# Kernel optimization log

Measured on AMD Instinct MI355X. Metric: run time of the kernel, lower is better.

Reference implementation:

```python
import jax, jax.numpy as jnp
import numpy as np

N_NODES, N_EDGES, IN_DIM, HID, N_FEAT_CLOSE, N_GRAPHS = 100000, 1600000, 128, 64, 5, 512


def _glorot(k, shape):
    lim = float(np.sqrt(6.0 / (shape[0] + shape[1])))
    return jax.random.uniform(k, shape, jnp.float32, -lim, lim)


def setup_inputs() -> dict:
    key = jax.random.key(0)
    ks = jax.random.split(key, 16)
    x = jax.random.normal(ks[0], (N_NODES, IN_DIM), jnp.float32)
    edge_index = jax.random.randint(ks[1], (2, N_EDGES), 0, N_NODES, jnp.int32)
    closeness = jax.random.uniform(ks[2], (N_NODES, N_FEAT_CLOSE), jnp.float32)
    batch = jnp.sort(jax.random.randint(ks[3], (N_NODES,), 0, N_GRAPHS, jnp.int32))
    return {
        'x': x, 'edge_index': edge_index, 'closeness': closeness, 'batch': batch,
        'num_graphs': N_GRAPHS,
        'W1': _glorot(ks[4], (IN_DIM, HID)), 'b1': jnp.zeros((HID,), jnp.float32),
        'W2': _glorot(ks[5], (HID, HID)), 'b2': jnp.zeros((HID,), jnp.float32),
        'W3': _glorot(ks[6], (HID, HID)), 'b3': jnp.zeros((HID,), jnp.float32),
        'Wc': _glorot(ks[7], (N_FEAT_CLOSE, 1)), 'bc': jnp.zeros((1,), jnp.float32),
        'Wa1': _glorot(ks[8], (HID, 16)), 'ba1': jnp.zeros((16,), jnp.float32),
        'Wa2': _glorot(ks[9], (16, 1)), 'ba2': jnp.zeros((1,), jnp.float32),
    }


def reference(x, edge_index, closeness, batch, num_graphs, W1, b1, W2, b2, W3, b3, Wc, bc, Wa1, ba1, Wa2, ba2):
    src, dst = edge_index[0], edge_index[1]
    N = x.shape[0]
    # GCN symmetric normalization with implicit self-loops (weight 1)
    deg = jax.ops.segment_sum(jnp.ones(src.shape, x.dtype), dst, num_segments=N) + 1.0
    dinv = jax.lax.rsqrt(deg)
    norm = dinv[src] * dinv[dst]  # [E]
    self_norm = (dinv * dinv)[:, None]  # 1/deg, self-loop coefficient

    def gcn(h, W, b):
        h = h @ W  # [N, hid]
        agg = jax.ops.segment_sum(h[src] * norm[:, None], dst, num_segments=N)
        return jax.nn.relu(agg + h * self_norm + b)

    h = gcn(x, W1, b1)
    h = gcn(h, W2, b2)
    h = gcn(h, W3, b3)

    # per-graph softmax over closeness scores, scaled by graph size
    s = closeness @ Wc + bc  # [N,1]
    smax = jax.ops.segment_max(s, batch, num_segments=num_graphs)
    e = jnp.exp(s - smax[batch])
    ssum = jax.ops.segment_sum(e, batch, num_segments=num_graphs)
    counts = jax.ops.segment_sum(jnp.ones((N,), x.dtype), batch, num_segments=num_graphs)
    w = (e / ssum[batch]) * counts[batch][:, None]  # [N,1]

    # weighted per-graph max pooling, then tiny MLP per graph
    pooled = jax.ops.segment_max(w * h, batch, num_segments=num_graphs)  # [G,64]
    a = jax.nn.relu(pooled @ Wa1 + ba1)
    return a @ Wa2 + ba2  # [G,1]
```

## Files before the change

### kernel.cpp

```cpp
#include <hip/hip_runtime.h>

#define N_NODESC 100000
#define N_EDGESC 1600000
#define IN_DIMC 128
#define HIDC 64
#define N_GRAPHSC 512
#define PAD_DEG 64


__global__ void zero_bounds_kernel(int* __restrict__ cntR, const int* __restrict__ batch,
                                   int* __restrict__ gstart) {
  int i = blockIdx.x * blockDim.x + threadIdx.x;
  if (i >= N_NODESC) return;
  cntR[i] = 0;
  cntR[N_NODESC + i] = 0;
  cntR[2 * N_NODESC + i] = 0;
  cntR[3 * N_NODESC + i] = 0;
  int b = batch[i];
  int prev = (i == 0) ? -1 : batch[i - 1];
  for (int g = prev + 1; g <= b; ++g) gstart[g] = i;
  if (i == N_NODESC - 1)
    for (int g = b + 1; g <= N_GRAPHSC; ++g) gstart[g] = N_NODESC;
}

__global__ void deg_kernel(const int* __restrict__ dstv, int* __restrict__ cntR,
                           int* __restrict__ slot) {
  int e4 = (blockIdx.x * blockDim.x + threadIdx.x) * 4;
  if (e4 >= N_EDGESC) return;
  int4 d = *(const int4*)(dstv + e4);
  int4 s;
  s.x = atomicAdd(&cntR[d.x], 1);
  s.y = atomicAdd(&cntR[N_NODESC + d.y], 1);
  s.z = atomicAdd(&cntR[2 * N_NODESC + d.z], 1);
  s.w = atomicAdd(&cntR[3 * N_NODESC + d.w], 1);
  *(int4*)(slot + e4) = s;
}

__global__ void off_dinv_kernel(const int* __restrict__ cntR, int* __restrict__ offR,
                                int* __restrict__ cnt, float* __restrict__ dinv) {
  int i = blockIdx.x * blockDim.x + threadIdx.x;
  if (i >= N_NODESC) return;
  int c0 = cntR[i];
  int c1 = cntR[N_NODESC + i];
  int c2 = cntR[2 * N_NODESC + i];
  int c3 = cntR[3 * N_NODESC + i];
  offR[i] = c0;
  offR[N_NODESC + i] = c0 + c1;
  offR[2 * N_NODESC + i] = c0 + c1 + c2;
  int tot = c0 + c1 + c2 + c3;
  cnt[i] = tot;
  dinv[i] = rsqrtf((float)tot + 1.0f);
}

__global__ void fill_pad_kernel(const int* __restrict__ srcv, const int* __restrict__ dstv,
                                const int* __restrict__ slot, const int* __restrict__ offR,
                                int* __restrict__ csr_pad) {
  int e4 = (blockIdx.x * blockDim.x + threadIdx.x) * 4;
  if (e4 >= N_EDGESC) return;
  int4 s = *(const int4*)(srcv + e4);
  int4 d = *(const int4*)(dstv + e4);
  int4 sl = *(const int4*)(slot + e4);
  int p0 = sl.x;
  int p1 = offR[d.y] + sl.y;
  int p2 = offR[N_NODESC + d.z] + sl.z;
  int p3 = offR[2 * N_NODESC + d.w] + sl.w;
  if (p0 < PAD_DEG) __builtin_nontemporal_store(s.x, &csr_pad[d.x * PAD_DEG + p0]);
  if (p1 < PAD_DEG) __builtin_nontemporal_store(s.y, &csr_pad[d.y * PAD_DEG + p1]);
  if (p2 < PAD_DEG) __builtin_nontemporal_store(s.z, &csr_pad[d.z * PAD_DEG + p2]);
  if (p3 < PAD_DEG) __builtin_nontemporal_store(s.w, &csr_pad[d.w * PAD_DEG + p3]);
}


#define GT_M 128
#define XS_LD 132
#define GT_BLOCKS ((N_NODESC + GT_M - 1) / GT_M)

template <int KT>
__global__ void __launch_bounds__(256, 3)
gemm_tile_kernel(const float* __restrict__ X, const float* __restrict__ W,
                 const float* __restrict__ dinv, float* __restrict__ T) {
  __shared__ float xs[64 * XS_LD];
  __shared__ float ws[64 * 64];
  int t = threadIdx.x;
  int base = blockIdx.x * GT_M;
  int r0 = (t >> 4) * 8;
  int c0 = (t & 15) * 4;
  float acc[8][4];
#pragma unroll
  for (int i = 0; i < 8; ++i)
#pragma unroll
    for (int j = 0; j < 4; ++j) acc[i][j] = 0.f;

  int kq = (t & 15) * 4;
  int rr = t >> 4;

  for (int kb = 0; kb < KT; kb += 64) {
    if (kb) __syncthreads();
#pragma unroll
    for (int it = 0; it < 8; ++it) {
      int r = rr + it * 16;
      int grow = base + r;
      if (grow >= N_NODESC) grow = N_NODESC - 1;
      float4 q = *(const float4*)(X + (size_t)grow * KT + kb + kq);
      xs[(kq + 0) * XS_LD + r] = q.x;
      xs[(kq + 1) * XS_LD + r] = q.y;
      xs[(kq + 2) * XS_LD + r] = q.z;
      xs[(kq + 3) * XS_LD + r] = q.w;
    }
#pragma unroll
    for (int it = 0; it < 4; ++it) {
      int idx = (it * 256 + t) * 4;
      *(float4*)(ws + idx) = *(const float4*)(W + (size_t)kb * HIDC + idx);
    }
    __syncthreads();
#pragma unroll 8
    for (int k = 0; k < 64; ++k) {
      float4 xa = *(const float4*)(xs + k * XS_LD + r0);
      float4 xb = *(const float4*)(xs + k * XS_LD + r0 + 4);
      float4 wf = *(const float4*)(ws + k * 64 + c0);
      float xf[8] = {xa.x, xa.y, xa.z, xa.w, xb.x, xb.y, xb.z, xb.w};
      float wv[4] = {wf.x, wf.y, wf.z, wf.w};
#pragma unroll
      for (int i = 0; i < 8; ++i)
#pragma unroll
        for (int j = 0; j < 4; ++j) acc[i][j] = fmaf(xf[i], wv[j], acc[i][j]);
    }
  }
#pragma unroll
  for (int i = 0; i < 8; ++i) {
    int row = base + r0 + i;
    if (row < N_NODESC) {
      float dv = dinv[row];
      float4 o;
      o.x = acc[i][0] * dv;
      o.y = acc[i][1] * dv;
      o.z = acc[i][2] * dv;
      o.w = acc[i][3] * dv;
      *(float4*)(T + (size_t)row * HIDC + c0) = o;
    }
  }
}

__global__ void gather_kernel(const float* __restrict__ ts, const float* __restrict__ dinv,
                              const int* __restrict__ cnt, const int* __restrict__ csr_pad,
                              const float* __restrict__ bias, float* __restrict__ h) {
  int lane = threadIdx.x & 63;
  int node = (blockIdx.x * blockDim.x + threadIdx.x) >> 6;
  if (node >= N_NODESC) return;
  int q = lane >> 4;
  int c = lane & 15;
  int deg = min(cnt[node], PAD_DEG);
  const int* __restrict__ row = csr_pad + node * PAD_DEG;
  const float4* __restrict__ ts4 = (const float4*)ts;
  float4 acc = make_float4(0.f, 0.f, 0.f, 0.f);
  int e = 0;
  for (; e + 16 <= deg; e += 16) {
    int s0 = row[e + q];
    int s1 = row[e + 4 + q];
    int s2 = row[e + 8 + q];
    int s3 = row[e + 12 + q];
    float4 v0 = ts4[s0 * 16 + c];
    float4 v1 = ts4[s1 * 16 + c];
    float4 v2 = ts4[s2 * 16 + c];
    float4 v3 = ts4[s3 * 16 + c];
    acc.x += (v0.x + v1.x) + (v2.x + v3.x);
    acc.y += (v0.y + v1.y) + (v2.y + v3.y);
    acc.z += (v0.z + v1.z) + (v2.z + v3.z);
    acc.w += (v0.w + v1.w) + (v2.w + v3.w);
  }
  for (; e + 4 <= deg; e += 4) {
    int s0 = row[e + q];
    float4 v = ts4[s0 * 16 + c];
    acc.x += v.x;
    acc.y += v.y;
    acc.z += v.z;
    acc.w += v.w;
  }
  if (e < deg && q < deg - e) {
    int s0 = row[e + q];
    float4 v = ts4[s0 * 16 + c];
    acc.x += v.x;
    acc.y += v.y;
    acc.z += v.z;
    acc.w += v.w;
  }
  acc.x += __shfl_xor(acc.x, 16);
  acc.y += __shfl_xor(acc.y, 16);
  acc.z += __shfl_xor(acc.z, 16);
  acc.w += __shfl_xor(acc.w, 16);
  acc.x += __shfl_xor(acc.x, 32);
  acc.y += __shfl_xor(acc.y, 32);
  acc.z += __shfl_xor(acc.z, 32);
  acc.w += __shfl_xor(acc.w, 32);
  if (q == 0) {
    float4 self = ts4[node * 16 + c];
    float4 bv = ((const float4*)bias)[c];
    float dv = dinv[node];
    float4 o;
    o.x = fmaxf(fmaf(acc.x + self.x, dv, bv.x), 0.f);
    o.y = fmaxf(fmaf(acc.y + self.y, dv, bv.y), 0.f);
    o.z = fmaxf(fmaf(acc.z + self.z, dv, bv.z), 0.f);
    o.w = fmaxf(fmaf(acc.w + self.w, dv, bv.w), 0.f);
    ((float4*)h)[node * 16 + c] = o;
  }
}

__global__ void __launch_bounds__(256)
readout_kernel(const float* __restrict__ h, const float* __restrict__ closeness,
               const float* __restrict__ Wc, const float* __restrict__ bc,
               const int* __restrict__ gstart, const float* __restrict__ Wa1,
               const float* __restrict__ ba1, const float* __restrict__ Wa2,
               const float* __restrict__ ba2, float* __restrict__ out) {
  __shared__ float sArr[1024];
  __shared__ float red[256];
  __shared__ float cross[4 * 64];
  int g = blockIdx.x;
  int t = threadIdx.x;
  int n0 = gstart[g], n1 = gstart[g + 1];
  int count = n1 - n0;
  int cap = min(count, 1024);
  float wc0 = Wc[0], wc1 = Wc[1], wc2 = Wc[2], wc3 = Wc[3], wc4 = Wc[4], bcv = bc[0];
  float lmax = -3.4e38f;
  for (int idx = t; idx < cap; idx += 256) {
    const float* c = closeness + (size_t)(n0 + idx) * 5;
    float s = fmaf(c[4], wc4, fmaf(c[3], wc3, fmaf(c[2], wc2, fmaf(c[1], wc1, fmaf(c[0], wc0, bcv)))));
    sArr[idx] = s;
    lmax = fmaxf(lmax, s);
  }
  red[t] = lmax;
  __syncthreads();
  for (int s = 128; s > 0; s >>= 1) {
    if (t < s) red[t] = fmaxf(red[t], red[t + s]);
    __syncthreads();
  }
  float m = red[0];
  __syncthreads();
  float lsum = 0.f;
  for (int idx = t; idx < cap; idx += 256) {
    float e = expf(sArr[idx] - m);
    sArr[idx] = e;
    lsum += e;
  }
  red[t] = lsum;
  __syncthreads();
  for (int s = 128; s > 0; s >>= 1) {
    if (t < s) red[t] += red[t + s];
    __syncthreads();
  }
  float scale = (count > 0) ? ((float)count / red[0]) : 0.f;
  __syncthreads();
  int wv = t >> 6, lane = t & 63;
  float pmax = 0.f;
  for (int idx = wv; idx < cap; idx += 4) {
    float w = sArr[idx] * scale;
    pmax = fmaxf(pmax, w * h[(size_t)(n0 + idx) * HIDC + lane]);
  }
  cross[wv * 64 + lane] = pmax;
  __syncthreads();
  if (wv == 0) {
    float p = fmaxf(fmaxf(cross[lane], cross[64 + lane]),
                    fmaxf(cross[128 + lane], cross[192 + lane]));
    float o = 0.f;
#pragma unroll
    for (int tt = 0; tt < 16; ++tt) {
      float prod = p * Wa1[lane * 16 + tt];
#pragma unroll
      for (int off = 32; off > 0; off >>= 1) prod += __shfl_xor(prod, off);
      float a = fmaxf(prod + ba1[tt], 0.f);
      o += a * Wa2[tt];
    }
    if (lane == 0) out[g] = o + ba2[0];
  }
}


extern "C" void kernel_launch(void* const* d_in, const int* in_sizes, int n_in,
                              void* d_out, int out_size, void* d_ws, size_t ws_size,
                              hipStream_t stream) {
  const float* x = (const float*)d_in[0];
  const int* ei = (const int*)d_in[1];
  const float* closeness = (const float*)d_in[2];
  const int* batch = (const int*)d_in[3];
  const float* W1 = (const float*)d_in[5];
  const float* b1 = (const float*)d_in[6];
  const float* W2 = (const float*)d_in[7];
  const float* b2 = (const float*)d_in[8];
  const float* W3 = (const float*)d_in[9];
  const float* b3 = (const float*)d_in[10];
  const float* Wc = (const float*)d_in[11];
  const float* bc = (const float*)d_in[12];
  const float* Wa1 = (const float*)d_in[13];
  const float* ba1 = (const float*)d_in[14];
  const float* Wa2 = (const float*)d_in[15];
  const float* ba2 = (const float*)d_in[16];
  float* out = (float*)d_out;
  const int* srcv = ei;
  const int* dstv = ei + N_EDGESC;

  char* ws = (char*)d_ws;
  size_t off = 0;
  auto alloc = [&](size_t bytes) -> void* {
    void* p = ws + off;
    off = (off + bytes + 255) & ~(size_t)255;
    return p;
  };
  float* tbuf = (float*)alloc(sizeof(float) * N_NODESC * HIDC);
  float* hbuf = (float*)alloc(sizeof(float) * N_NODESC * HIDC);
  int* csr_pad = (int*)alloc(sizeof(int) * N_NODESC * PAD_DEG);
  int* slot = (int*)alloc(sizeof(int) * N_EDGESC);
  int* cntR = (int*)alloc(sizeof(int) * N_NODESC * 4);
  int* offR = (int*)alloc(sizeof(int) * N_NODESC * 3);
  int* cnt = (int*)alloc(sizeof(int) * N_NODESC);
  float* dinv = (float*)alloc(sizeof(float) * N_NODESC);
  int* gstart = (int*)alloc(sizeof(int) * (N_GRAPHSC + 1));

  const int B = 256;
  int gN = (N_NODESC + B - 1) / B;
  int gE4 = (N_EDGESC / 4 + B - 1) / B;
  int gGather = (N_NODESC * 64) / B;

  zero_bounds_kernel<<<gN, B, 0, stream>>>(cntR, batch, gstart);
  deg_kernel<<<gE4, B, 0, stream>>>(dstv, cntR, slot);
  off_dinv_kernel<<<gN, B, 0, stream>>>(cntR, offR, cnt, dinv);
  fill_pad_kernel<<<gE4, B, 0, stream>>>(srcv, dstv, slot, offR, csr_pad);

  gemm_tile_kernel<IN_DIMC><<<GT_BLOCKS, B, 0, stream>>>(x, W1, dinv, tbuf);
  gather_kernel<<<gGather, B, 0, stream>>>(tbuf, dinv, cnt, csr_pad, b1, hbuf);
  gemm_tile_kernel<HIDC><<<GT_BLOCKS, B, 0, stream>>>(hbuf, W2, dinv, tbuf);
  gather_kernel<<<gGather, B, 0, stream>>>(tbuf, dinv, cnt, csr_pad, b2, hbuf);
  gemm_tile_kernel<HIDC><<<GT_BLOCKS, B, 0, stream>>>(hbuf, W3, dinv, tbuf);
  gather_kernel<<<gGather, B, 0, stream>>>(tbuf, dinv, cnt, csr_pad, b3, hbuf);

  readout_kernel<<<N_GRAPHSC, B, 0, stream>>>(hbuf, closeness, Wc, bc, gstart,
                                              Wa1, ba1, Wa2, ba2, out);
}
```

Baseline: 517.0 us.

## Build CSR in one pass with four interleaved per-replica padded segments

```diff
diff --git a/kernel.cpp b/kernel.cpp
--- a/kernel.cpp
+++ b/kernel.cpp
@@ -5,7 +5,12 @@
 #define IN_DIMC 128
 #define HIDC 64
 #define N_GRAPHSC 512
-#define PAD_DEG 64
+
+#define PAD_SEG 20
+#define ROW_INTS (4 * PAD_SEG)
+
+typedef int v4i __attribute__((ext_vector_type(4)));
+typedef float v4f __attribute__((ext_vector_type(4)));
 
 
 __global__ void zero_bounds_kernel(int* __restrict__ cntR, const int* __restrict__ batch,
@@ -23,51 +28,31 @@
     for (int g = b + 1; g <= N_GRAPHSC; ++g) gstart[g] = N_NODESC;
 }
 
-__global__ void deg_kernel(const int* __restrict__ dstv, int* __restrict__ cntR,
-                           int* __restrict__ slot) {
+__global__ void build_kernel(const int* __restrict__ srcv, const int* __restrict__ dstv,
+                             int* __restrict__ cntR, int* __restrict__ csr_pad) {
   int e4 = (blockIdx.x * blockDim.x + threadIdx.x) * 4;
   if (e4 >= N_EDGESC) return;
-  int4 d = *(const int4*)(dstv + e4);
-  int4 s;
-  s.x = atomicAdd(&cntR[d.x], 1);
-  s.y = atomicAdd(&cntR[N_NODESC + d.y], 1);
-  s.z = atomicAdd(&cntR[2 * N_NODESC + d.z], 1);
-  s.w = atomicAdd(&cntR[3 * N_NODESC + d.w], 1);
-  *(int4*)(slot + e4) = s;
-}
-
-__global__ void off_dinv_kernel(const int* __restrict__ cntR, int* __restrict__ offR,
-                                int* __restrict__ cnt, float* __restrict__ dinv) {
+  v4i s = __builtin_nontemporal_load((const v4i*)(srcv + e4));
+  v4i d = __builtin_nontemporal_load((const v4i*)(dstv + e4));
+  int p0 = atomicAdd(&cntR[d[0]], 1);
+  int p1 = atomicAdd(&cntR[N_NODESC + d[1]], 1);
+  int p2 = atomicAdd(&cntR[2 * N_NODESC + d[2]], 1);
+  int p3 = atomicAdd(&cntR[3 * N_NODESC + d[3]], 1);
+  if (p0 < PAD_SEG)
+    __builtin_nontemporal_store(s[0], &csr_pad[d[0] * ROW_INTS + (p0 >> 2) * 16 + 0 + (p0 & 3)]);
+  if (p1 < PAD_SEG)
+    __builtin_nontemporal_store(s[1], &csr_pad[d[1] * ROW_INTS + (p1 >> 2) * 16 + 4 + (p1 & 3)]);
+  if (p2 < PAD_SEG)
+    __builtin_nontemporal_store(s[2], &csr_pad[d[2] * ROW_INTS + (p2 >> 2) * 16 + 8 + (p2 & 3)]);
+  if (p3 < PAD_SEG)
+    __builtin_nontemporal_store(s[3], &csr_pad[d[3] * ROW_INTS + (p3 >> 2) * 16 + 12 + (p3 & 3)]);
+}
+
+__global__ void dinv_kernel(const int* __restrict__ cntR, float* __restrict__ dinv) {
   int i = blockIdx.x * blockDim.x + threadIdx.x;
   if (i >= N_NODESC) return;
-  int c0 = cntR[i];
-  int c1 = cntR[N_NODESC + i];
-  int c2 = cntR[2 * N_NODESC + i];
-  int c3 = cntR[3 * N_NODESC + i];
-  offR[i] = c0;
-  offR[N_NODESC + i] = c0 + c1;
-  offR[2 * N_NODESC + i] = c0 + c1 + c2;
-  int tot = c0 + c1 + c2 + c3;
-  cnt[i] = tot;
+  int tot = cntR[i] + cntR[N_NODESC + i] + cntR[2 * N_NODESC + i] + cntR[3 * N_NODESC + i];
   dinv[i] = rsqrtf((float)tot + 1.0f);
-}
-
-__global__ void fill_pad_kernel(const int* __restrict__ srcv, const int* __restrict__ dstv,
-                                const int* __restrict__ slot, const int* __restrict__ offR,
-                                int* __restrict__ csr_pad) {
-  int e4 = (blockIdx.x * blockDim.x + threadIdx.x) * 4;
-  if (e4 >= N_EDGESC) return;
-  int4 s = *(const int4*)(srcv + e4);
-  int4 d = *(const int4*)(dstv + e4);
-  int4 sl = *(const int4*)(slot + e4);
-  int p0 = sl.x;
-  int p1 = offR[d.y] + sl.y;
-  int p2 = offR[N_NODESC + d.z] + sl.z;
-  int p3 = offR[2 * N_NODESC + d.w] + sl.w;
-  if (p0 < PAD_DEG) __builtin_nontemporal_store(s.x, &csr_pad[d.x * PAD_DEG + p0]);
-  if (p1 < PAD_DEG) __builtin_nontemporal_store(s.y, &csr_pad[d.y * PAD_DEG + p1]);
-  if (p2 < PAD_DEG) __builtin_nontemporal_store(s.z, &csr_pad[d.z * PAD_DEG + p2]);
-  if (p3 < PAD_DEG) __builtin_nontemporal_store(s.w, &csr_pad[d.w * PAD_DEG + p3]);
 }
 
 
@@ -142,47 +127,34 @@
 }
 
 __global__ void gather_kernel(const float* __restrict__ ts, const float* __restrict__ dinv,
-                              const int* __restrict__ cnt, const int* __restrict__ csr_pad,
+                              const int* __restrict__ cntR, const int* __restrict__ csr_pad,
                               const float* __restrict__ bias, float* __restrict__ h) {
   int lane = threadIdx.x & 63;
   int node = (blockIdx.x * blockDim.x + threadIdx.x) >> 6;
   if (node >= N_NODESC) return;
   int q = lane >> 4;
   int c = lane & 15;
-  int deg = min(cnt[node], PAD_DEG);
-  const int* __restrict__ row = csr_pad + node * PAD_DEG;
+  int cq = min(cntR[q * N_NODESC + node], PAD_SEG);
+  const int* __restrict__ rowp = csr_pad + node * ROW_INTS;
   const float4* __restrict__ ts4 = (const float4*)ts;
   float4 acc = make_float4(0.f, 0.f, 0.f, 0.f);
-  int e = 0;
-  for (; e + 16 <= deg; e += 16) {
-    int s0 = row[e + q];
-    int s1 = row[e + 4 + q];
-    int s2 = row[e + 8 + q];
-    int s3 = row[e + 12 + q];
-    float4 v0 = ts4[s0 * 16 + c];
-    float4 v1 = ts4[s1 * 16 + c];
-    float4 v2 = ts4[s2 * 16 + c];
-    float4 v3 = ts4[s3 * 16 + c];
-    acc.x += (v0.x + v1.x) + (v2.x + v3.x);
-    acc.y += (v0.y + v1.y) + (v2.y + v3.y);
-    acc.z += (v0.z + v1.z) + (v2.z + v3.z);
-    acc.w += (v0.w + v1.w) + (v2.w + v3.w);
-  }
-  for (; e + 4 <= deg; e += 4) {
-    int s0 = row[e + q];
-    float4 v = ts4[s0 * 16 + c];
-    acc.x += v.x;
-    acc.y += v.y;
-    acc.z += v.z;
-    acc.w += v.w;
-  }
-  if (e < deg && q < deg - e) {
-    int s0 = row[e + q];
-    float4 v = ts4[s0 * 16 + c];
-    acc.x += v.x;
-    acc.y += v.y;
-    acc.z += v.z;
-    acc.w += v.w;
+  for (int kb = 0; kb * 4 < cq; ++kb) {
+    v4i s4 = __builtin_nontemporal_load((const v4i*)(rowp + kb * 16 + q * 4));
+    int b = kb * 4;
+    float4 v0 = ts4[s4[0] * 16 + c];
+    acc.x += v0.x; acc.y += v0.y; acc.z += v0.z; acc.w += v0.w;
+    if (b + 1 < cq) {
+      float4 v = ts4[s4[1] * 16 + c];
+      acc.x += v.x; acc.y += v.y; acc.z += v.z; acc.w += v.w;
+    }
+    if (b + 2 < cq) {
+      float4 v = ts4[s4[2] * 16 + c];
+      acc.x += v.x; acc.y += v.y; acc.z += v.z; acc.w += v.w;
+    }
+    if (b + 3 < cq) {
+      float4 v = ts4[s4[3] * 16 + c];
+      acc.x += v.x; acc.y += v.y; acc.z += v.z; acc.w += v.w;
+    }
   }
   acc.x += __shfl_xor(acc.x, 16);
   acc.y += __shfl_xor(acc.y, 16);
@@ -196,12 +168,12 @@
     float4 self = ts4[node * 16 + c];
     float4 bv = ((const float4*)bias)[c];
     float dv = dinv[node];
-    float4 o;
-    o.x = fmaxf(fmaf(acc.x + self.x, dv, bv.x), 0.f);
-    o.y = fmaxf(fmaf(acc.y + self.y, dv, bv.y), 0.f);
-    o.z = fmaxf(fmaf(acc.z + self.z, dv, bv.z), 0.f);
-    o.w = fmaxf(fmaf(acc.w + self.w, dv, bv.w), 0.f);
-    ((float4*)h)[node * 16 + c] = o;
+    v4f o;
+    o[0] = fmaxf(fmaf(acc.x + self.x, dv, bv.x), 0.f);
+    o[1] = fmaxf(fmaf(acc.y + self.y, dv, bv.y), 0.f);
+    o[2] = fmaxf(fmaf(acc.z + self.z, dv, bv.z), 0.f);
+    o[3] = fmaxf(fmaf(acc.w + self.w, dv, bv.w), 0.f);
+    __builtin_nontemporal_store(o, (v4f*)h + node * 16 + c);
   }
 }
 
@@ -306,11 +278,8 @@
   };
   float* tbuf = (float*)alloc(sizeof(float) * N_NODESC * HIDC);
   float* hbuf = (float*)alloc(sizeof(float) * N_NODESC * HIDC);
-  int* csr_pad = (int*)alloc(sizeof(int) * N_NODESC * PAD_DEG);
-  int* slot = (int*)alloc(sizeof(int) * N_EDGESC);
+  int* csr_pad = (int*)alloc(sizeof(int) * N_NODESC * ROW_INTS);
   int* cntR = (int*)alloc(sizeof(int) * N_NODESC * 4);
-  int* offR = (int*)alloc(sizeof(int) * N_NODESC * 3);
-  int* cnt = (int*)alloc(sizeof(int) * N_NODESC);
   float* dinv = (float*)alloc(sizeof(float) * N_NODESC);
   int* gstart = (int*)alloc(sizeof(int) * (N_GRAPHSC + 1));
 
@@ -320,16 +289,15 @@
   int gGather = (N_NODESC * 64) / B;
 
   zero_bounds_kernel<<<gN, B, 0, stream>>>(cntR, batch, gstart);
-  deg_kernel<<<gE4, B, 0, stream>>>(dstv, cntR, slot);
-  off_dinv_kernel<<<gN, B, 0, stream>>>(cntR, offR, cnt, dinv);
-  fill_pad_kernel<<<gE4, B, 0, stream>>>(srcv, dstv, slot, offR, csr_pad);
+  build_kernel<<<gE4, B, 0, stream>>>(srcv, dstv, cntR, csr_pad);
+  dinv_kernel<<<gN, B, 0, stream>>>(cntR, dinv);
 
   gemm_tile_kernel<IN_DIMC><<<GT_BLOCKS, B, 0, stream>>>(x, W1, dinv, tbuf);
-  gather_kernel<<<gGather, B, 0, stream>>>(tbuf, dinv, cnt, csr_pad, b1, hbuf);
+  gather_kernel<<<gGather, B, 0, stream>>>(tbuf, dinv, cntR, csr_pad, b1, hbuf);
   gemm_tile_kernel<HIDC><<<GT_BLOCKS, B, 0, stream>>>(hbuf, W2, dinv, tbuf);
-  gather_kernel<<<gGather, B, 0, stream>>>(tbuf, dinv, cnt, csr_pad, b2, hbuf);
+  gather_kernel<<<gGather, B, 0, stream>>>(tbuf, dinv, cntR, csr_pad, b2, hbuf);
   gemm_tile_kernel<HIDC><<<GT_BLOCKS, B, 0, stream>>>(hbuf, W3, dinv, tbuf);
-  gather_kernel<<<gGather, B, 0, stream>>>(tbuf, dinv, cnt, csr_pad, b3, hbuf);
+  gather_kernel<<<gGather, B, 0, stream>>>(tbuf, dinv, cntR, csr_pad, b3, hbuf);
 
   readout_kernel<<<N_GRAPHSC, B, 0, stream>>>(hbuf, closeness, Wc, bc, gstart,
                                               Wa1, ba1, Wa2, ba2, out);
```

New measurement: 577.6 us. +11.7%, slower.

## Replace tiled GEMM with per-wave split-K GEMM and smem reduction

Applied to the files above, without the earlier changes.

```diff
diff --git a/kernel.cpp b/kernel.cpp
--- a/kernel.cpp
+++ b/kernel.cpp
@@ -70,73 +70,110 @@
   if (p3 < PAD_DEG) __builtin_nontemporal_store(s.w, &csr_pad[d.w * PAD_DEG + p3]);
 }
 
-
 #define GT_M 128
-#define XS_LD 132
 #define GT_BLOCKS ((N_NODESC + GT_M - 1) / GT_M)
 
 template <int KT>
-__global__ void __launch_bounds__(256, 3)
-gemm_tile_kernel(const float* __restrict__ X, const float* __restrict__ W,
-                 const float* __restrict__ dinv, float* __restrict__ T) {
-  __shared__ float xs[64 * XS_LD];
-  __shared__ float ws[64 * 64];
-  int t = threadIdx.x;
+__global__ void __launch_bounds__(128, 1)
+gemm_split_kernel(const float* __restrict__ X, const float* __restrict__ W,
+                  const float* __restrict__ dinv, float* __restrict__ T) {
+  constexpr int KHALF = KT / 2;
+  constexpr int NROUND = KHALF / 32;
+  __shared__ float smem[2 * 32 * 128 + 2 * 32 * 64];
+  int tid = threadIdx.x;
+  int w = tid >> 6;
+  int l = tid & 63;
+  float* __restrict__ xs = smem + w * (32 * 128);
+  float* __restrict__ ws = smem + 2 * 32 * 128 + w * (32 * 64);
   int base = blockIdx.x * GT_M;
-  int r0 = (t >> 4) * 8;
-  int c0 = (t & 15) * 4;
-  float acc[8][4];
+
+  int kq = (l & 7) * 4;
+  int rg = (l >> 3) * 4;
+  int r0 = (l >> 2) * 8;
+  int c0 = (l & 3) * 16;
+
+  float4 acc[8][4];
 #pragma unroll
   for (int i = 0; i < 8; ++i)
 #pragma unroll
-    for (int j = 0; j < 4; ++j) acc[i][j] = 0.f;
-
-  int kq = (t & 15) * 4;
-  int rr = t >> 4;
-
-  for (int kb = 0; kb < KT; kb += 64) {
-    if (kb) __syncthreads();
-#pragma unroll
-    for (int it = 0; it < 8; ++it) {
-      int r = rr + it * 16;
-      int grow = base + r;
-      if (grow >= N_NODESC) grow = N_NODESC - 1;
-      float4 q = *(const float4*)(X + (size_t)grow * KT + kb + kq);
-      xs[(kq + 0) * XS_LD + r] = q.x;
-      xs[(kq + 1) * XS_LD + r] = q.y;
-      xs[(kq + 2) * XS_LD + r] = q.z;
-      xs[(kq + 3) * XS_LD + r] = q.w;
-    }
-#pragma unroll
-    for (int it = 0; it < 4; ++it) {
-      int idx = (it * 256 + t) * 4;
-      *(float4*)(ws + idx) = *(const float4*)(W + (size_t)kb * HIDC + idx);
-    }
-    __syncthreads();
-#pragma unroll 8
-    for (int k = 0; k < 64; ++k) {
-      float4 xa = *(const float4*)(xs + k * XS_LD + r0);
-      float4 xb = *(const float4*)(xs + k * XS_LD + r0 + 4);
-      float4 wf = *(const float4*)(ws + k * 64 + c0);
+    for (int j = 0; j < 4; ++j) acc[i][j] = make_float4(0.f, 0.f, 0.f, 0.f);
+
+  for (int t = 0; t < NROUND; ++t) {
+    int kb = w * KHALF + t * 32;
+#pragma unroll
+    for (int p = 0; p < 4; ++p) {
+      int r = p * 32 + rg;
+      int row0 = base + r;
+      float4 v0 = *(const float4*)(X + (size_t)min(row0 + 0, N_NODESC - 1) * KT + kb + kq);
+      float4 v1 = *(const float4*)(X + (size_t)min(row0 + 1, N_NODESC - 1) * KT + kb + kq);
+      float4 v2 = *(const float4*)(X + (size_t)min(row0 + 2, N_NODESC - 1) * KT + kb + kq);
+      float4 v3 = *(const float4*)(X + (size_t)min(row0 + 3, N_NODESC - 1) * KT + kb + kq);
+      const float* a0 = (const float*)&v0;
+      const float* a1 = (const float*)&v1;
+      const float* a2 = (const float*)&v2;
+      const float* a3 = (const float*)&v3;
+#pragma unroll
+      for (int i = 0; i < 4; ++i) {
+        float4 xw = make_float4(a0[i], a1[i], a2[i], a3[i]);
+        *(float4*)(xs + (kq + i) * 128 + r) = xw;
+      }
+    }
+#pragma unroll
+    for (int j = 0; j < 8; ++j) {
+      int f = j * 64 + l;
+      int kl = f >> 4;
+      int c4 = (f & 15) * 4;
+      *(float4*)(ws + kl * 64 + c4) = *(const float4*)(W + (size_t)(kb + kl) * HIDC + c4);
+    }
+#pragma unroll 4
+    for (int k = 0; k < 32; ++k) {
+      float4 xa = *(const float4*)(xs + k * 128 + r0);
+      float4 xb = *(const float4*)(xs + k * 128 + r0 + 4);
+      float4 w0 = *(const float4*)(ws + k * 64 + c0);
+      float4 w1 = *(const float4*)(ws + k * 64 + c0 + 4);
+      float4 w2 = *(const float4*)(ws + k * 64 + c0 + 8);
+      float4 w3 = *(const float4*)(ws + k * 64 + c0 + 12);
       float xf[8] = {xa.x, xa.y, xa.z, xa.w, xb.x, xb.y, xb.z, xb.w};
-      float wv[4] = {wf.x, wf.y, wf.z, wf.w};
+      float4 wv[4] = {w0, w1, w2, w3};
 #pragma unroll
       for (int i = 0; i < 8; ++i)
 #pragma unroll
-        for (int j = 0; j < 4; ++j) acc[i][j] = fmaf(xf[i], wv[j], acc[i][j]);
-    }
-  }
-#pragma unroll
-  for (int i = 0; i < 8; ++i) {
-    int row = base + r0 + i;
-    if (row < N_NODESC) {
-      float dv = dinv[row];
-      float4 o;
-      o.x = acc[i][0] * dv;
-      o.y = acc[i][1] * dv;
-      o.z = acc[i][2] * dv;
-      o.w = acc[i][3] * dv;
-      *(float4*)(T + (size_t)row * HIDC + c0) = o;
+        for (int j = 0; j < 4; ++j) {
+          acc[i][j].x = fmaf(xf[i], wv[j].x, acc[i][j].x);
+          acc[i][j].y = fmaf(xf[i], wv[j].y, acc[i][j].y);
+          acc[i][j].z = fmaf(xf[i], wv[j].z, acc[i][j].z);
+          acc[i][j].w = fmaf(xf[i], wv[j].w, acc[i][j].w);
+        }
+    }
+  }
+
+  float* __restrict__ scratch = smem;
+  __syncthreads();
+  if (w == 1) {
+#pragma unroll
+    for (int i = 0; i < 8; ++i)
+#pragma unroll
+      for (int j = 0; j < 4; ++j)
+        *(float4*)(scratch + (i * 4 + j) * 256 + l * 4) = acc[i][j];
+  }
+  __syncthreads();
+  if (w == 0) {
+#pragma unroll
+    for (int i = 0; i < 8; ++i) {
+      int row = base + r0 + i;
+      if (row < N_NODESC) {
+        float dv = dinv[row];
+#pragma unroll
+        for (int j = 0; j < 4; ++j) {
+          float4 s = *(const float4*)(scratch + (i * 4 + j) * 256 + l * 4);
+          float4 o;
+          o.x = (acc[i][j].x + s.x) * dv;
+          o.y = (acc[i][j].y + s.y) * dv;
+          o.z = (acc[i][j].z + s.z) * dv;
+          o.w = (acc[i][j].w + s.w) * dv;
+          *(float4*)(T + (size_t)row * HIDC + c0 + 4 * j) = o;
+        }
+      }
     }
   }
 }
@@ -324,11 +361,11 @@
   off_dinv_kernel<<<gN, B, 0, stream>>>(cntR, offR, cnt, dinv);
   fill_pad_kernel<<<gE4, B, 0, stream>>>(srcv, dstv, slot, offR, csr_pad);
 
-  gemm_tile_kernel<IN_DIMC><<<GT_BLOCKS, B, 0, stream>>>(x, W1, dinv, tbuf);
+  gemm_split_kernel<IN_DIMC><<<GT_BLOCKS, 128, 0, stream>>>(x, W1, dinv, tbuf);
   gather_kernel<<<gGather, B, 0, stream>>>(tbuf, dinv, cnt, csr_pad, b1, hbuf);
-  gemm_tile_kernel<HIDC><<<GT_BLOCKS, B, 0, stream>>>(hbuf, W2, dinv, tbuf);
+  gemm_split_kernel<HIDC><<<GT_BLOCKS, 128, 0, stream>>>(hbuf, W2, dinv, tbuf);
   gather_kernel<<<gGather, B, 0, stream>>>(tbuf, dinv, cnt, csr_pad, b2, hbuf);
-  gemm_tile_kernel<HIDC><<<GT_BLOCKS, B, 0, stream>>>(hbuf, W3, dinv, tbuf);
+  gemm_split_kernel<HIDC><<<GT_BLOCKS, 128, 0, stream>>>(hbuf, W3, dinv, tbuf);
   gather_kernel<<<gGather, B, 0, stream>>>(tbuf, dinv, cnt, csr_pad, b3, hbuf);
 
   readout_kernel<<<N_GRAPHSC, B, 0, stream>>>(hbuf, closeness, Wc, bc, gstart,
```

After: 538.5 us. 4.2% more time.

## Retile node GEMM to 8x16 register blocks with 16-wide K chunks

Applied to the files above, without the earlier changes.

```diff
diff --git a/kernel.cpp b/kernel.cpp
--- a/kernel.cpp
+++ b/kernel.cpp
@@ -70,60 +70,76 @@
   if (p3 < PAD_DEG) __builtin_nontemporal_store(s.w, &csr_pad[d.w * PAD_DEG + p3]);
 }
 
-
-#define GT_M 128
-#define XS_LD 132
-#define GT_BLOCKS ((N_NODESC + GT_M - 1) / GT_M)
+#define GR_M 256
+#define GR_KC 16
+#define XS_STRIDE 288
+#define GR_BLOCKS ((N_NODESC + GR_M - 1) / GR_M)
+
+__device__ __forceinline__ int pcol(int r) { return r + 4 * (r >> 5); }
 
 template <int KT>
-__global__ void __launch_bounds__(256, 3)
-gemm_tile_kernel(const float* __restrict__ X, const float* __restrict__ W,
-                 const float* __restrict__ dinv, float* __restrict__ T) {
-  __shared__ float xs[64 * XS_LD];
-  __shared__ float ws[64 * 64];
+__global__ void __launch_bounds__(128, 2)
+gemm_rc_kernel(const float* __restrict__ X, const float* __restrict__ W,
+               const float* __restrict__ dinv, float* __restrict__ T) {
+  __shared__ float xs[GR_KC * XS_STRIDE];
+  __shared__ float ws[GR_KC * 64];
   int t = threadIdx.x;
-  int base = blockIdx.x * GT_M;
-  int r0 = (t >> 4) * 8;
-  int c0 = (t & 15) * 4;
-  float acc[8][4];
+  int base = blockIdx.x * GR_M;
+  int rg = t >> 2;
+  int cg = t & 3;
+  int r0 = rg * 8;
+  int c0 = cg * 16;
+  int kq = cg * 4;
+  int px = pcol(r0);
+
+  float4 acc[8][4];
 #pragma unroll
   for (int i = 0; i < 8; ++i)
 #pragma unroll
-    for (int j = 0; j < 4; ++j) acc[i][j] = 0.f;
-
-  int kq = (t & 15) * 4;
-  int rr = t >> 4;
-
-  for (int kb = 0; kb < KT; kb += 64) {
+    for (int j = 0; j < 4; ++j) acc[i][j] = make_float4(0.f, 0.f, 0.f, 0.f);
+
+  for (int kb = 0; kb < KT; kb += GR_KC) {
     if (kb) __syncthreads();
-#pragma unroll
-    for (int it = 0; it < 8; ++it) {
-      int r = rr + it * 16;
-      int grow = base + r;
-      if (grow >= N_NODESC) grow = N_NODESC - 1;
-      float4 q = *(const float4*)(X + (size_t)grow * KT + kb + kq);
-      xs[(kq + 0) * XS_LD + r] = q.x;
-      xs[(kq + 1) * XS_LD + r] = q.y;
-      xs[(kq + 2) * XS_LD + r] = q.z;
-      xs[(kq + 3) * XS_LD + r] = q.w;
-    }
-#pragma unroll
-    for (int it = 0; it < 4; ++it) {
-      int idx = (it * 256 + t) * 4;
-      *(float4*)(ws + idx) = *(const float4*)(W + (size_t)kb * HIDC + idx);
+    float4 xv[8];
+#pragma unroll
+    for (int i = 0; i < 8; ++i) {
+      int row = base + r0 + i;
+      if (row >= N_NODESC) row = N_NODESC - 1;
+      xv[i] = *(const float4*)(X + (size_t)row * KT + kb + kq);
+    }
+#pragma unroll
+    for (int c = 0; c < 4; ++c) {
+      const float* a = (const float*)xv;
+      float4 w0 = make_float4(a[0 * 4 + c], a[1 * 4 + c], a[2 * 4 + c], a[3 * 4 + c]);
+      float4 w1 = make_float4(a[4 * 4 + c], a[5 * 4 + c], a[6 * 4 + c], a[7 * 4 + c]);
+      *(float4*)(xs + (kq + c) * XS_STRIDE + px) = w0;
+      *(float4*)(xs + (kq + c) * XS_STRIDE + px + 4) = w1;
+    }
+#pragma unroll
+    for (int j = 0; j < 2; ++j) {
+      int f = t * 2 + j;
+      int kl = f >> 4;
+      int c4 = (f & 15) * 4;
+      *(float4*)(ws + kl * 64 + c4) = *(const float4*)(W + (size_t)(kb + kl) * HIDC + c4);
     }
     __syncthreads();
-#pragma unroll 8
-    for (int k = 0; k < 64; ++k) {
-      float4 xa = *(const float4*)(xs + k * XS_LD + r0);
-      float4 xb = *(const float4*)(xs + k * XS_LD + r0 + 4);
-      float4 wf = *(const float4*)(ws + k * 64 + c0);
+#pragma unroll
+    for (int k = 0; k < GR_KC; ++k) {
+      float4 xa = *(const float4*)(xs + k * XS_STRIDE + px);
+      float4 xb = *(const float4*)(xs + k * XS_STRIDE + px + 4);
+      float4 wv[4];
+#pragma unroll
+      for (int j = 0; j < 4; ++j) wv[j] = *(const float4*)(ws + k * 64 + c0 + 4 * j);
       float xf[8] = {xa.x, xa.y, xa.z, xa.w, xb.x, xb.y, xb.z, xb.w};
-      float wv[4] = {wf.x, wf.y, wf.z, wf.w};
 #pragma unroll
       for (int i = 0; i < 8; ++i)
 #pragma unroll
-        for (int j = 0; j < 4; ++j) acc[i][j] = fmaf(xf[i], wv[j], acc[i][j]);
+        for (int j = 0; j < 4; ++j) {
+          acc[i][j].x = fmaf(xf[i], wv[j].x, acc[i][j].x);
+          acc[i][j].y = fmaf(xf[i], wv[j].y, acc[i][j].y);
+          acc[i][j].z = fmaf(xf[i], wv[j].z, acc[i][j].z);
+          acc[i][j].w = fmaf(xf[i], wv[j].w, acc[i][j].w);
+        }
     }
   }
 #pragma unroll
@@ -131,12 +147,15 @@
     int row = base + r0 + i;
     if (row < N_NODESC) {
       float dv = dinv[row];
-      float4 o;
-      o.x = acc[i][0] * dv;
-      o.y = acc[i][1] * dv;
-      o.z = acc[i][2] * dv;
-      o.w = acc[i][3] * dv;
-      *(float4*)(T + (size_t)row * HIDC + c0) = o;
+#pragma unroll
+      for (int j = 0; j < 4; ++j) {
+        float4 o;
+        o.x = acc[i][j].x * dv;
+        o.y = acc[i][j].y * dv;
+        o.z = acc[i][j].z * dv;
+        o.w = acc[i][j].w * dv;
+        *(float4*)(T + (size_t)row * HIDC + c0 + 4 * j) = o;
+      }
     }
   }
 }
@@ -324,11 +343,11 @@
   off_dinv_kernel<<<gN, B, 0, stream>>>(cntR, offR, cnt, dinv);
   fill_pad_kernel<<<gE4, B, 0, stream>>>(srcv, dstv, slot, offR, csr_pad);
 
-  gemm_tile_kernel<IN_DIMC><<<GT_BLOCKS, B, 0, stream>>>(x, W1, dinv, tbuf);
+  gemm_rc_kernel<IN_DIMC><<<GR_BLOCKS, 128, 0, stream>>>(x, W1, dinv, tbuf);
   gather_kernel<<<gGather, B, 0, stream>>>(tbuf, dinv, cnt, csr_pad, b1, hbuf);
-  gemm_tile_kernel<HIDC><<<GT_BLOCKS, B, 0, stream>>>(hbuf, W2, dinv, tbuf);
+  gemm_rc_kernel<HIDC><<<GR_BLOCKS, 128, 0, stream>>>(hbuf, W2, dinv, tbuf);
   gather_kernel<<<gGather, B, 0, stream>>>(tbuf, dinv, cnt, csr_pad, b2, hbuf);
-  gemm_tile_kernel<HIDC><<<GT_BLOCKS, B, 0, stream>>>(hbuf, W3, dinv, tbuf);
+  gemm_rc_kernel<HIDC><<<GR_BLOCKS, 128, 0, stream>>>(hbuf, W3, dinv, tbuf);
   gather_kernel<<<gGather, B, 0, stream>>>(tbuf, dinv, cnt, csr_pad, b3, hbuf);
 
   readout_kernel<<<N_GRAPHSC, B, 0, stream>>>(hbuf, closeness, Wc, bc, gstart,
```

After: 555.0 us. 1.07x slower.
